# Kernel tuning notes

Hardware: AMD Instinct MI355X
Metric: run time of the kernel (lower is better)

The kernel has to match this reference:

```python
import jax, jax.numpy as jnp
import numpy as np

B, N, H = 4, 256, 512
P = 128  # game_physics_params


def _init(key, shape, scale=0.02):
    return jax.random.normal(key, shape, dtype=jnp.float32) * scale


def setup_inputs() -> dict:
    key = jax.random.key(0)
    ks = jax.random.split(key, 16)
    return {
        "object_features": jax.random.normal(ks[0], (B, N, H), dtype=jnp.float32),
        # physics_predictor: H -> 512 -> P
        "pp_w1": _init(ks[1], (H, 512)), "pp_b1": jnp.zeros((512,), jnp.float32),
        "pp_w2": _init(ks[2], (512, P)), "pp_b2": jnp.zeros((P,), jnp.float32),
        # collision_detector: 2H -> 256 -> 128 -> 1
        "cd_w1": _init(ks[3], (2 * H, 256)), "cd_b1": jnp.zeros((256,), jnp.float32),
        "cd_w2": _init(ks[4], (256, 128)), "cd_b2": jnp.zeros((128,), jnp.float32),
        "cd_w3": _init(ks[5], (128, 1)), "cd_b3": jnp.zeros((1,), jnp.float32),
        # velocity / force heads: H -> 3
        "vel_w": _init(ks[6], (H, 3)), "vel_b": jnp.zeros((3,), jnp.float32),
        "frc_w": _init(ks[7], (H, 3)), "frc_b": jnp.zeros((3,), jnp.float32),
    }


def reference(object_features, pp_w1, pp_b1, pp_w2, pp_b2,
              cd_w1, cd_b1, cd_w2, cd_b2, cd_w3, cd_b3,
              vel_w, vel_b, frc_w, frc_b):
    x = object_features  # [B, N, H]
    # physics predictor MLP
    p = jax.nn.relu(x @ pp_w1 + pp_b1) @ pp_w2 + pp_b2  # [B, N, P]
    mass = jax.nn.sigmoid(p[..., 0:1]) * 100.0
    friction = jax.nn.sigmoid(p[..., 1:2])
    elasticity = jax.nn.sigmoid(p[..., 2:3])
    density = jax.nn.sigmoid(p[..., 3:4]) * 10.0
    velocities = x @ vel_w + vel_b  # [B, N, 3]
    forces = x @ frc_w + frc_b      # [B, N, 3]

    # vectorized pairwise collision detection over upper-triangle pairs
    iu, ju = np.triu_indices(N, k=1)  # static index arrays, length Np = N(N-1)/2
    pairs = jnp.concatenate([x[:, iu], x[:, ju]], axis=-1)  # [B, Np, 2H]
    h = jax.nn.relu(pairs @ cd_w1 + cd_b1)
    h = jax.nn.relu(h @ cd_w2 + cd_b2)
    prob = jax.nn.sigmoid(h @ cd_w3 + cd_b3)[..., 0]  # [B, Np]
    collision_matrix = jnp.zeros((x.shape[0], N, N), dtype=x.dtype)
    collision_matrix = collision_matrix.at[:, iu, ju].set(prob).at[:, ju, iu].set(prob)

    return (mass, friction, elasticity, density, velocities, forces, collision_matrix)
```

## Files before the change

kernel.cpp:

```cpp
#include <hip/hip_runtime.h>
#include <hip/hip_bf16.h>

typedef __attribute__((ext_vector_type(8))) short bf16x8;
typedef __attribute__((ext_vector_type(4))) float f32x4;

__device__ __forceinline__ float sigmoidf_(float v) {
    return 1.0f / (1.0f + __expf(-v));
}
__device__ __forceinline__ short f2bf(float f) {
    union { __hip_bfloat16 h; short s; } cv;
    cv.h = __float2bfloat16(f);
    return cv.s;
}
__device__ __forceinline__ float bf2f(short s) {
    union { float f; unsigned u; } cv;
    cv.u = ((unsigned)(unsigned short)s) << 16;
    return cv.f;
}

__global__ __launch_bounds__(256) void convert_kernel(
    const float* __restrict__ x, const float* __restrict__ pp_w1,
    const float* __restrict__ cd_w1, const float* __restrict__ cd_w2,
    const float* __restrict__ pp_w2, const float* __restrict__ vel_w,
    const float* __restrict__ frc_w,
    __hip_bfloat16* __restrict__ xb, __hip_bfloat16* __restrict__ Wt,
    __hip_bfloat16* __restrict__ w2t, float* __restrict__ hw)
{
    __shared__ float ts[64][65];
    const int b = blockIdx.x, t = threadIdx.x;

    if (b < 256) {
        int base = b * 2048 + t * 8;
        float4 a = *(const float4*)(x + base);
        float4 c = *(const float4*)(x + base + 4);
        bf16x8 o;
        o[0] = f2bf(a.x); o[1] = f2bf(a.y); o[2] = f2bf(a.z); o[3] = f2bf(a.w);
        o[4] = f2bf(c.x); o[5] = f2bf(c.y); o[6] = f2bf(c.z); o[7] = f2bf(c.w);
        *(bf16x8*)(xb + base) = o;
        return;
    }
    if (b == 392) {
        for (int e = t; e < 5120; e += 256) {
            int h = e >> 9, k = e & 511;
            float v = (h < 4) ? pp_w2[k * 128 + h]
                    : (h < 7) ? vel_w[k * 3 + (h - 4)]
                              : frc_w[k * 3 + (h - 7)];
            hw[e] = v;
        }
        return;
    }

    const float* src; int ss, k0, n0, region;
    if (b < 320)      { int i = b - 256; src = pp_w1; ss = 512; k0 = (i >> 3) * 64; n0 = (i & 7) * 64; region = 0; }
    else if (b < 384) { int i = b - 320; src = cd_w1; ss = 256; k0 = (i >> 2) * 64; n0 = (i & 3) * 64; region = 1; }
    else              { int i = b - 384; src = cd_w2; ss = 128; k0 = (i >> 1) * 64; n0 = (i & 1) * 64; region = 2; }

    #pragma unroll
    for (int i = 0; i < 4; ++i) {
        int r = (t >> 4) + i * 16, c4 = (t & 15) * 4;
        *(float4*)&ts[r][c4] = *(const float4*)(src + (k0 + r) * ss + n0 + c4);
    }
    __syncthreads();
    #pragma unroll
    for (int i = 0; i < 4; ++i) {
        int nOut = (t >> 4) + i * 16, kc = (t & 15) * 4;
        ushort4 o;
        o.x = (unsigned short)f2bf(ts[kc + 0][nOut]);
        o.y = (unsigned short)f2bf(ts[kc + 1][nOut]);
        o.z = (unsigned short)f2bf(ts[kc + 2][nOut]);
        o.w = (unsigned short)f2bf(ts[kc + 3][nOut]);
        int gn = n0 + nOut, gk = k0 + kc;
        if (region == 0)      *(ushort4*)(Wt + gn * 512 + gk) = o;
        else if (region == 1) {
            int row = (gk < 512) ? (512 + gn) : (768 + gn);
            *(ushort4*)(Wt + row * 512 + (gk & 511)) = o;
        } else                *(ushort4*)(w2t + gn * 256 + gk) = o;
    }
}

__global__ __launch_bounds__(256) void gemm_kernel(
    const __hip_bfloat16* __restrict__ xb, const __hip_bfloat16* __restrict__ Wt,
    const float* __restrict__ pp_b1, const float* __restrict__ cd_b1,
    __hip_bfloat16* __restrict__ hidg, __hip_bfloat16* __restrict__ Ugb,
    __hip_bfloat16* __restrict__ Vgb)
{
    const int t = threadIdx.x;
    const int wave = t >> 6, lane = t & 63;
    const int l = lane & 15, q = lane >> 4;
    const int m0 = blockIdx.x * 32;
    const int n0 = blockIdx.y * 128 + wave * 32;

    const __hip_bfloat16* a0p = xb + (m0 + l) * 512 + q * 8;
    const __hip_bfloat16* a1p = a0p + 16 * 512;
    const __hip_bfloat16* b0p = Wt + (n0 + l) * 512 + q * 8;
    const __hip_bfloat16* b1p = b0p + 16 * 512;

    f32x4 acc00 = {}, acc01 = {}, acc10 = {}, acc11 = {};
    #pragma unroll
    for (int ks = 0; ks < 16; ++ks) {
        bf16x8 a0 = *(const bf16x8*)(a0p + ks * 32);
        bf16x8 a1 = *(const bf16x8*)(a1p + ks * 32);
        bf16x8 b0 = *(const bf16x8*)(b0p + ks * 32);
        bf16x8 b1 = *(const bf16x8*)(b1p + ks * 32);
        acc00 = __builtin_amdgcn_mfma_f32_16x16x32_bf16(a0, b0, acc00, 0, 0, 0);
        acc01 = __builtin_amdgcn_mfma_f32_16x16x32_bf16(a0, b1, acc01, 0, 0, 0);
        acc10 = __builtin_amdgcn_mfma_f32_16x16x32_bf16(a1, b0, acc10, 0, 0, 0);
        acc11 = __builtin_amdgcn_mfma_f32_16x16x32_bf16(a1, b1, acc11, 0, 0, 0);
    }

    const int c0 = n0 + l, c1 = n0 + 16 + l;
    #pragma unroll
    for (int mt = 0; mt < 2; ++mt) {
        const f32x4& A0 = mt ? acc10 : acc00;
        const f32x4& A1 = mt ? acc11 : acc01;
        if (n0 < 512) {
            float b0v = pp_b1[c0], b1v = pp_b1[c1];
            #pragma unroll
            for (int r = 0; r < 4; ++r) {
                int rg = m0 + mt * 16 + q * 4 + r;
                hidg[rg * 512 + c0] = __float2bfloat16(fmaxf(A0[r] + b0v, 0.f));
                hidg[rg * 512 + c1] = __float2bfloat16(fmaxf(A1[r] + b1v, 0.f));
            }
        } else if (n0 < 768) {
            float b0v = cd_b1[c0 - 512], b1v = cd_b1[c1 - 512];
            #pragma unroll
            for (int r = 0; r < 4; ++r) {
                int rg = m0 + mt * 16 + q * 4 + r;
                Ugb[rg * 256 + (c0 - 512)] = __float2bfloat16(A0[r] + b0v);
                Ugb[rg * 256 + (c1 - 512)] = __float2bfloat16(A1[r] + b1v);
            }
        } else {
            #pragma unroll
            for (int r = 0; r < 4; ++r) {
                int rg = m0 + mt * 16 + q * 4 + r;
                Vgb[rg * 256 + (c0 - 768)] = __float2bfloat16(A0[r]);
                Vgb[rg * 256 + (c1 - 768)] = __float2bfloat16(A1[r]);
            }
        }
    }
}

__global__ __launch_bounds__(128, 3) void pair_kernel(
    const __hip_bfloat16* __restrict__ Ugb, const __hip_bfloat16* __restrict__ Vgb,
    const __hip_bfloat16* __restrict__ w2t,
    const float* __restrict__ cd_b2, const float* __restrict__ cd_w3,
    const float* __restrict__ cd_b3, float* __restrict__ cm,
    const float* __restrict__ x, const __hip_bfloat16* __restrict__ hidg,
    const float* __restrict__ hw, const float* __restrict__ pp_b2,
    const float* __restrict__ vel_b, const float* __restrict__ frc_b,
    float* __restrict__ out)
{
    __shared__ __align__(16) char lds[8320];

    const int t = threadIdx.x;
    const int wave = t >> 6, lane = t & 63;
    const int bx = blockIdx.x;

    if (bx >= 2112) {
        const int row0 = (bx - 2112) * 16 + wave * 8;
        for (int rr = 0; rr < 8; ++rr) {
            const int row = row0 + rr;
            const float4* xr = (const float4*)(x + row * 512);
            float4 xa = xr[lane * 2], xc = xr[lane * 2 + 1];
            bf16x8 hb = *(const bf16x8*)(hidg + row * 512 + lane * 8);
            float hf[8];
            #pragma unroll
            for (int j = 0; j < 8; ++j) hf[j] = bf2f(hb[j]);

            #pragma unroll
            for (int h = 0; h < 10; ++h) {
                const float4* wr = (const float4*)(hw + h * 512);
                float4 wa = wr[lane * 2], wc = wr[lane * 2 + 1];
                float s;
                if (h < 4) {
                    s = hf[0]*wa.x + hf[1]*wa.y + hf[2]*wa.z + hf[3]*wa.w
                      + hf[4]*wc.x + hf[5]*wc.y + hf[6]*wc.z + hf[7]*wc.w;
                } else {
                    s = xa.x*wa.x + xa.y*wa.y + xa.z*wa.z + xa.w*wa.w
                      + xc.x*wc.x + xc.y*wc.y + xc.z*wc.z + xc.w*wc.w;
                }
                s += __shfl_xor(s, 1);  s += __shfl_xor(s, 2);
                s += __shfl_xor(s, 4);  s += __shfl_xor(s, 8);
                s += __shfl_xor(s, 16); s += __shfl_xor(s, 32);
                if (lane == 0) {
                    if (h < 4) {
                        float sg = sigmoidf_(s + pp_b2[h]);
                        out[h * 1024 + row] = (h == 0) ? sg * 100.f : (h == 3) ? sg * 10.f : sg;
                    } else if (h < 7) {
                        out[4096 + row * 3 + (h - 4)] = s + vel_b[h - 4];
                    } else {
                        out[7168 + row * 3 + (h - 7)] = s + frc_b[h - 7];
                    }
                }
            }
        }
        return;
    }

    const int tp = bx >> 2, u = bx & 3;
    int ti = (int)((65.0f - sqrtf(4225.0f - 8.0f * (float)tp)) * 0.5f);
    while ((ti + 1) * (65 - (ti + 1)) / 2 <= tp) ++ti;
    while (ti * (65 - ti) / 2 > tp) --ti;
    const int tj = ti + (tp - ti * (65 - ti) / 2);
    const int i0 = ti * 8, j0 = tj * 8;

    const int l = lane & 15, q = lane >> 4;

    {
        const __hip_bfloat16* src = (wave == 0)
            ? (Ugb + ((u << 8) + i0) * 256)
            : (Vgb + ((u << 8) + j0) * 256);
        char* dst = lds + wave * 4160;
        #pragma unroll
        for (int c = 0; c < 4; ++c) {
            __builtin_amdgcn_global_load_lds(
                (const __attribute__((address_space(1))) void*)(src + c * 512),
                (__attribute__((address_space(3))) void*)(dst + c * 1040), 16, 0, 0);
        }
    }

    float b2v[8], w3v[8];
    #pragma unroll
    for (int nt = 0; nt < 8; ++nt) {
        b2v[nt] = cd_b2[nt * 16 + l];
        w3v[nt] = cd_w3[nt * 16 + l];
    }
    const float b3 = cd_b3[0];

    __syncthreads();

    f32x4 acc[2][8];
    #pragma unroll
    for (int mt = 0; mt < 2; ++mt)
        #pragma unroll
        for (int nt = 0; nt < 8; ++nt)
            acc[mt][nt] = (f32x4){0.f, 0.f, 0.f, 0.f};

    const int vrow = l & 7;
    const char* Vb = lds + 4160 + (vrow >> 1) * 1040 + (vrow & 1) * 512;

    #pragma unroll 2
    for (int ks = 0; ks < 8; ++ks) {
        const int koff = ks * 64 + q * 16;
        bf16x8 bfr[8];
        #pragma unroll
        for (int nt = 0; nt < 8; ++nt)
            bfr[nt] = *(const bf16x8*)(w2t + (nt * 16 + l) * 256 + ks * 32 + q * 8);
        #pragma unroll
        for (int mt = 0; mt < 2; ++mt) {
            const int urow = (wave << 2) + (mt << 1) + (l >> 3);
            bf16x8 ub = *(const bf16x8*)(lds + (urow >> 1) * 1040 + (urow & 1) * 512 + koff);
            bf16x8 vb = *(const bf16x8*)(Vb + koff);
            bf16x8 afr;
            #pragma unroll
            for (int j = 0; j < 8; ++j)
                afr[j] = f2bf(fmaxf(bf2f(ub[j]) + bf2f(vb[j]), 0.f));
            #pragma unroll
            for (int nt = 0; nt < 8; ++nt)
                acc[mt][nt] = __builtin_amdgcn_mfma_f32_16x16x32_bf16(afr, bfr[nt], acc[mt][nt], 0, 0, 0);
        }
    }

    float* base = cm + u * 65536;
    #pragma unroll
    for (int mt = 0; mt < 2; ++mt) {
        #pragma unroll
        for (int r = 0; r < 4; ++r) {
            float s = 0.f;
            #pragma unroll
            for (int nt = 0; nt < 8; ++nt)
                s += fmaxf(acc[mt][nt][r] + b2v[nt], 0.f) * w3v[nt];
            s += __shfl_xor(s, 1);
            s += __shfl_xor(s, 2);
            s += __shfl_xor(s, 4);
            s += __shfl_xor(s, 8);
            if (l == 0) {
                const int p = (wave << 5) + (mt << 4) + (q << 2) + r;
                const int i = i0 + (p >> 3), j = j0 + (p & 7);
                float prob = 1.0f / (1.0f + __expf(-(s + b3)));
                if (i < j) {
                    base[i * 256 + j] = prob;
                    base[j * 256 + i] = prob;
                } else if (i == j) {
                    base[i * 256 + i] = 0.0f;
                }
            }
        }
    }
}

extern "C" void kernel_launch(void* const* d_in, const int* in_sizes, int n_in,
                              void* d_out, int out_size, void* d_ws, size_t ws_size,
                              hipStream_t stream) {
    const float* x     = (const float*)d_in[0];
    const float* pp_w1 = (const float*)d_in[1];
    const float* pp_b1 = (const float*)d_in[2];
    const float* pp_w2 = (const float*)d_in[3];
    const float* pp_b2 = (const float*)d_in[4];
    const float* cd_w1 = (const float*)d_in[5];
    const float* cd_b1 = (const float*)d_in[6];
    const float* cd_w2 = (const float*)d_in[7];
    const float* cd_b2 = (const float*)d_in[8];
    const float* cd_w3 = (const float*)d_in[9];
    const float* cd_b3 = (const float*)d_in[10];
    const float* vel_w = (const float*)d_in[11];
    const float* vel_b = (const float*)d_in[12];
    const float* frc_w = (const float*)d_in[13];
    const float* frc_b = (const float*)d_in[14];

    float* out = (float*)d_out;
    __hip_bfloat16* Ugb  = (__hip_bfloat16*)d_ws;
    __hip_bfloat16* Vgb  = Ugb + 262144;
    __hip_bfloat16* xb   = Vgb + 262144;
    __hip_bfloat16* Wt   = xb + 524288;
    __hip_bfloat16* hidg = Wt + 524288;
    __hip_bfloat16* w2t  = hidg + 524288;
    float* hw = (float*)(w2t + 32768);

    convert_kernel<<<dim3(393), dim3(256), 0, stream>>>(
        x, pp_w1, cd_w1, cd_w2, pp_w2, vel_w, frc_w, xb, Wt, w2t, hw);
    gemm_kernel<<<dim3(32, 8), dim3(256), 0, stream>>>(
        xb, Wt, pp_b1, cd_b1, hidg, Ugb, Vgb);
    pair_kernel<<<dim3(2176), dim3(128), 0, stream>>>(
        Ugb, Vgb, w2t, cd_b2, cd_w3, cd_b3, out + 10240,
        x, hidg, hw, pp_b2, vel_b, frc_b, out);
}
```

Before: 149.2 us.

## Load U/V pair tiles directly from global memory instead of staging through LDS

The pair kernel no longer stages the U and V row tiles in shared memory with global_load_lds and a barrier. Each lane now reads its bf16x8 fragments straight from global or L2, shares the V conversion between the two M tiles, and fully unrolls the K loop. Launch bounds drop from 3 to 2 blocks per SIMD to give the compiler more registers. This removes the LDS round trip and the __syncthreads, but relies on caches to absorb the repeated global reads and may lower occupancy.

After: 157.0 us. 5.3% more time.

```diff
diff --git a/kernel.cpp b/kernel.cpp
--- a/kernel.cpp
+++ b/kernel.cpp
@@ -140,7 +140,7 @@
     }
 }
 
-__global__ __launch_bounds__(128, 3) void pair_kernel(
+__global__ __launch_bounds__(128, 2) void pair_kernel(
     const __hip_bfloat16* __restrict__ Ugb, const __hip_bfloat16* __restrict__ Vgb,
     const __hip_bfloat16* __restrict__ w2t,
     const float* __restrict__ cd_b2, const float* __restrict__ cd_w3,
@@ -150,8 +150,6 @@
     const float* __restrict__ vel_b, const float* __restrict__ frc_b,
     float* __restrict__ out)
 {
-    __shared__ __align__(16) char lds[8320];
-
     const int t = threadIdx.x;
     const int wave = t >> 6, lane = t & 63;
     const int bx = blockIdx.x;
@@ -206,18 +204,12 @@
 
     const int l = lane & 15, q = lane >> 4;
 
-    {
-        const __hip_bfloat16* src = (wave == 0)
-            ? (Ugb + ((u << 8) + i0) * 256)
-            : (Vgb + ((u << 8) + j0) * 256);
-        char* dst = lds + wave * 4160;
-        #pragma unroll
-        for (int c = 0; c < 4; ++c) {
-            __builtin_amdgcn_global_load_lds(
-                (const __attribute__((address_space(1))) void*)(src + c * 512),
-                (__attribute__((address_space(3))) void*)(dst + c * 1040), 16, 0, 0);
-        }
-    }
+    const __hip_bfloat16* Ubb = Ugb + ((u << 8) + i0) * 256;
+    const __hip_bfloat16* Vbb = Vgb + ((u << 8) + j0) * 256;
+    const __hip_bfloat16* ubase0 = Ubb + ((wave << 2) + 0 + (l >> 3)) * 256 + q * 8;
+    const __hip_bfloat16* ubase1 = Ubb + ((wave << 2) + 2 + (l >> 3)) * 256 + q * 8;
+    const __hip_bfloat16* vbase  = Vbb + (l & 7) * 256 + q * 8;
+    const __hip_bfloat16* wbase  = w2t + l * 256 + q * 8;
 
     float b2v[8], w3v[8];
     #pragma unroll
@@ -227,55 +219,53 @@
     }
     const float b3 = cd_b3[0];
 
-    __syncthreads();
-
     f32x4 acc[2][8];
     #pragma unroll
-    for (int mt = 0; mt < 2; ++mt)
+    for (int mth = 0; mth < 2; ++mth)
         #pragma unroll
         for (int nt = 0; nt < 8; ++nt)
-            acc[mt][nt] = (f32x4){0.f, 0.f, 0.f, 0.f};
-
-    const int vrow = l & 7;
-    const char* Vb = lds + 4160 + (vrow >> 1) * 1040 + (vrow & 1) * 512;
-
-    #pragma unroll 2
+            acc[mth][nt] = (f32x4){0.f, 0.f, 0.f, 0.f};
+
+    #pragma unroll
     for (int ks = 0; ks < 8; ++ks) {
-        const int koff = ks * 64 + q * 16;
+        const int ko = ks * 32;
         bf16x8 bfr[8];
         #pragma unroll
         for (int nt = 0; nt < 8; ++nt)
-            bfr[nt] = *(const bf16x8*)(w2t + (nt * 16 + l) * 256 + ks * 32 + q * 8);
-        #pragma unroll
-        for (int mt = 0; mt < 2; ++mt) {
-            const int urow = (wave << 2) + (mt << 1) + (l >> 3);
-            bf16x8 ub = *(const bf16x8*)(lds + (urow >> 1) * 1040 + (urow & 1) * 512 + koff);
-            bf16x8 vb = *(const bf16x8*)(Vb + koff);
-            bf16x8 afr;
-            #pragma unroll
-            for (int j = 0; j < 8; ++j)
-                afr[j] = f2bf(fmaxf(bf2f(ub[j]) + bf2f(vb[j]), 0.f));
-            #pragma unroll
-            for (int nt = 0; nt < 8; ++nt)
-                acc[mt][nt] = __builtin_amdgcn_mfma_f32_16x16x32_bf16(afr, bfr[nt], acc[mt][nt], 0, 0, 0);
-        }
+            bfr[nt] = *(const bf16x8*)(wbase + nt * 4096 + ko);
+        bf16x8 u0 = *(const bf16x8*)(ubase0 + ko);
+        bf16x8 u1 = *(const bf16x8*)(ubase1 + ko);
+        bf16x8 vv = *(const bf16x8*)(vbase + ko);
+        bf16x8 a0, a1;
+        #pragma unroll
+        for (int j = 0; j < 8; ++j) {
+            float vf = bf2f(vv[j]);
+            a0[j] = f2bf(fmaxf(bf2f(u0[j]) + vf, 0.f));
+            a1[j] = f2bf(fmaxf(bf2f(u1[j]) + vf, 0.f));
+        }
+        #pragma unroll
+        for (int nt = 0; nt < 8; ++nt)
+            acc[0][nt] = __builtin_amdgcn_mfma_f32_16x16x32_bf16(a0, bfr[nt], acc[0][nt], 0, 0, 0);
+        #pragma unroll
+        for (int nt = 0; nt < 8; ++nt)
+            acc[1][nt] = __builtin_amdgcn_mfma_f32_16x16x32_bf16(a1, bfr[nt], acc[1][nt], 0, 0, 0);
     }
 
     float* base = cm + u * 65536;
     #pragma unroll
-    for (int mt = 0; mt < 2; ++mt) {
+    for (int mth = 0; mth < 2; ++mth) {
         #pragma unroll
         for (int r = 0; r < 4; ++r) {
             float s = 0.f;
             #pragma unroll
             for (int nt = 0; nt < 8; ++nt)
-                s += fmaxf(acc[mt][nt][r] + b2v[nt], 0.f) * w3v[nt];
+                s += fmaxf(acc[mth][nt][r] + b2v[nt], 0.f) * w3v[nt];
             s += __shfl_xor(s, 1);
             s += __shfl_xor(s, 2);
             s += __shfl_xor(s, 4);
             s += __shfl_xor(s, 8);
             if (l == 0) {
-                const int p = (wave << 5) + (mt << 4) + (q << 2) + r;
+                const int p = ((wave << 1) + mth) * 16 + (q << 2) + r;
                 const int i = i0 + (p >> 3), j = j0 + (p & 7);
                 float prob = 1.0f / (1.0f + __expf(-(s + b3)));
                 if (i < j) {
```
